# Kernel tuning notes

Hardware: AMD Instinct MI355X
Metric: run time of the kernel (lower is better)

Reference implementation:

```python
import jax, jax.numpy as jnp
import numpy as np

B, S, D, H = 2, 2048, 1024, 16
HD = D // H  # head_dim = 64


def setup_inputs() -> dict:
    key = jax.random.key(0)
    ks = jax.random.split(key, 12)
    xav = (2.0 / (D + D)) ** 0.5  # xavier_normal std for square Linear
    q = jax.random.normal(ks[0], (B, S, D), jnp.float32)
    k = jax.random.normal(ks[1], (B, S, D), jnp.float32)
    v = jax.random.normal(ks[2], (B, S, D), jnp.float32)
    Wq = jax.random.normal(ks[3], (D, D), jnp.float32) * xav
    Wk = jax.random.normal(ks[4], (D, D), jnp.float32) * xav
    Wv = jax.random.normal(ks[5], (D, D), jnp.float32) * xav
    bq = jnp.zeros((D,), jnp.float32)
    bk = jnp.zeros((D,), jnp.float32)
    bv = jnp.zeros((D,), jnp.float32)
    # valid-prefix padding masks (True = valid token); key 0 always valid so
    # no causal softmax row is fully masked (avoids NaN, matches real usage).
    klen = jax.random.randint(ks[6], (B,), S // 2, S + 1)
    qlen = jax.random.randint(ks[7], (B,), S // 2, S + 1)
    pos = jnp.arange(S)
    key_padding_mask = pos[None, :] < klen[:, None]
    query_padding_mask = pos[None, :] < qlen[:, None]
    return {
        "q": q, "k": k, "v": v,
        "Wq": Wq, "bq": bq, "Wk": Wk, "bk": bk, "Wv": Wv, "bv": bv,
        "key_padding_mask": key_padding_mask,
        "query_padding_mask": query_padding_mask,
    }


def _proj_split(x, W, b, n_heads):
    # Linear (y = x W^T + b) then split heads: [B,S,D] -> [B,H,S,hd]
    bsz, sq, dm = x.shape
    hd = dm // n_heads
    y = x @ W.T + b
    return y.reshape(bsz, sq, n_heads, hd).transpose(0, 2, 1, 3)


def reference(q, k, v, Wq, bq, Wk, bk, Wv, bv, key_padding_mask, query_padding_mask):
    bsz, sq, dm = q.shape
    sk = k.shape[1]
    Q = _proj_split(q, Wq, bq, H)  # [B,H,Sq,hd]
    K = _proj_split(k, Wk, bk, H)  # [B,H,Sk,hd]
    V = _proj_split(v, Wv, bv, H)  # [B,H,Sk,hd]
    scale = 1.0 / jnp.sqrt(jnp.asarray(Q.shape[-1], Q.dtype))
    scores = jnp.einsum('bhqd,bhkd->bhqk', Q, K) * scale  # [B,H,Sq,Sk]
    # key padding: -inf where key invalid
    scores = jnp.where(key_padding_mask[:, None, None, :], scores, -jnp.inf)
    # causal: -inf strictly above the diagonal
    causal_ok = jnp.tril(jnp.ones((sq, sk), bool))
    scores = jnp.where(causal_ok[None, None, :, :], scores, -jnp.inf)
    attn = jax.nn.softmax(scores, axis=-1)
    # q_mask: zero out rows for padded queries (post-softmax, as in source)
    attn = jnp.where(query_padding_mask[:, None, :, None], attn, 0.0)
    # dropout p=0.0 -> identity
    out = jnp.einsum('bhqk,bhkd->bhqd', attn, V)
    out = out.transpose(0, 2, 1, 3).reshape(bsz, sq, dm)
    return out + q
```

## Files before the change

kernel.cpp:

```cpp
#include <hip/hip_runtime.h>
#include <stdint.h>

#define BATCH 2
#define SEQ 2048
#define DMODEL 1024
#define NHEAD 16
#define HDIM 64
#define CVT_BLOCKS 15360

typedef __attribute__((ext_vector_type(8))) short bf16x8;
typedef __attribute__((ext_vector_type(4))) float f32x4;

__device__ __forceinline__ unsigned short f2bf(float f) {
  unsigned int u = __float_as_uint(f);
  u += 0x7fffu + ((u >> 16) & 1u);
  return (unsigned short)(u >> 16);
}
__device__ __forceinline__ unsigned int pk2bf(float a, float b) {
  return __builtin_amdgcn_perm(__float_as_uint(b) + 0x8000u,
                               __float_as_uint(a) + 0x8000u, 0x07060302u);
}
__device__ __forceinline__ void async_copy16(const void* g, void* l) {
  __builtin_amdgcn_global_load_lds(
      (const __attribute__((address_space(1))) void*)g,
      (__attribute__((address_space(3))) void*)l, 16, 0, 0);
}

__global__ __launch_bounds__(256) void cvt_all(
    const float* __restrict__ q, const float* __restrict__ k,
    const float* __restrict__ v, const float* __restrict__ Wq,
    const float* __restrict__ Wk, const float* __restrict__ Wv,
    unsigned short* __restrict__ dst,
    const unsigned char* __restrict__ kp, const unsigned char* __restrict__ qp,
    int* __restrict__ lens) {
  if (blockIdx.x == CVT_BLOCKS) {
    const int t = threadIdx.x, wave = t >> 6, lane = t & 63;
    const unsigned char* base = (wave < 2) ? kp : qp;
    const int b = wave & 1;
    const bool bytefmt = (base[1] != 0);
    int cnt = 0;
    if (bytefmt) {
      const uint4* p = (const uint4*)(base + (size_t)b * SEQ);
#pragma unroll
      for (int g = 0; g < 2; g++) {
        const uint4 x = p[g * 64 + lane];
        const unsigned int w[4] = {x.x, x.y, x.z, x.w};
#pragma unroll
        for (int i = 0; i < 4; i++) {
          const unsigned int ww = w[i];
          cnt += ((ww & 0xffu) != 0) + ((ww & 0xff00u) != 0) +
                 ((ww & 0xff0000u) != 0) + ((ww & 0xff000000u) != 0);
        }
      }
    } else {
      const uint4* p = (const uint4*)(base + (size_t)b * SEQ * 4);
#pragma unroll
      for (int g = 0; g < 8; g++) {
        const uint4 x = p[g * 64 + lane];
        cnt += (x.x != 0) + (x.y != 0) + (x.z != 0) + (x.w != 0);
      }
    }
#pragma unroll
    for (int off = 32; off >= 1; off >>= 1) cnt += __shfl_xor(cnt, off, 64);
    if (lane == 0) lens[wave] = cnt;
    return;
  }
  const int g = blockIdx.x * 256 + threadIdx.x;
  const float* src;
  size_t off, dbase;
  if (g < 3 * (1 << 20)) {
    const int ti = g >> 20;
    src = (ti == 0) ? q : (ti == 1) ? k : v;
    off = (size_t)(g & ((1 << 20) - 1));
    dbase = (size_t)ti << 22;
  } else {
    const int gw = g - 3 * (1 << 20);
    const int ti = gw >> 18;
    src = (ti == 0) ? Wq : (ti == 1) ? Wk : Wv;
    off = (size_t)(gw & ((1 << 18) - 1));
    dbase = (3ull << 22) + ((size_t)ti << 20);
  }
  const float4 x = ((const float4*)src)[off];
  ushort4 o;
  o.x = f2bf(x.x); o.y = f2bf(x.y); o.z = f2bf(x.z); o.w = f2bf(x.w);
  *(ushort4*)(dst + dbase + off * 4) = o;
}

__global__ __launch_bounds__(256) void qkv_proj(
    const unsigned short* __restrict__ xq, const unsigned short* __restrict__ xk,
    const unsigned short* __restrict__ xv,
    const unsigned short* __restrict__ Wq, const float* __restrict__ bq,
    const unsigned short* __restrict__ Wk, const float* __restrict__ bk,
    const unsigned short* __restrict__ Wv, const float* __restrict__ bv,
    unsigned short* __restrict__ Qo, unsigned short* __restrict__ Ko,
    unsigned short* __restrict__ Vo, const int* __restrict__ lens) {
  const int z = blockIdx.z;
  const int m0 = blockIdx.y * 128, n0 = blockIdx.x * 128;
  const int b = m0 >> 11;
  const int len = (z == 0) ? lens[2 + b] : lens[b];
  if ((m0 & (SEQ - 1)) >= len) return;

  const unsigned short* x = (z == 0) ? xq : (z == 1) ? xk : xv;
  const unsigned short* W = (z == 0) ? Wq : (z == 1) ? Wk : Wv;
  const float* bias = (z == 0) ? bq : (z == 1) ? bk : bv;
  unsigned short* dst = (z == 0) ? Qo : (z == 1) ? Ko : Vo;
  const float osc = (z == 0) ? 0.18033688011112042f : 1.0f;

  __shared__ unsigned short As[128 * 64];
  __shared__ unsigned short Bs[128 * 64];

  const int t = threadIdx.x;
  const int wave = t >> 6, lane = t & 63, quad = lane >> 4, l16 = lane & 15;
  const int wm = wave >> 1, wn = wave & 1;

  const f32x4 fz = {0.f, 0.f, 0.f, 0.f};
  f32x4 acc[4][4];
#pragma unroll
  for (int i = 0; i < 4; i++)
#pragma unroll
    for (int j = 0; j < 4; j++) acc[i][j] = fz;

  for (int k0 = 0; k0 < DMODEL; k0 += 64) {
    __syncthreads();
#pragma unroll
    for (int c = 0; c < 4; c++) {
      const int slot = c * 256 + t;
      const int row = slot >> 3, pg = slot & 7;
      const int lg = (pg ^ (row & 7)) * 8;
      async_copy16(x + (size_t)(m0 + row) * DMODEL + k0 + lg,
                   (char*)As + (c * 256 + (t & 192)) * 16);
      async_copy16(W + (size_t)(n0 + row) * DMODEL + k0 + lg,
                   (char*)Bs + (c * 256 + (t & 192)) * 16);
    }
    __syncthreads();
#pragma unroll
    for (int kk = 0; kk < 2; kk++) {
      bf16x8 af[4], bfr[4];
#pragma unroll
      for (int i = 0; i < 4; i++) {
        const int ra = wm * 64 + i * 16 + l16;
        const int rb = wn * 64 + i * 16 + l16;
        af[i] = *(const bf16x8*)(As + ra * 64 + ((kk * 4 + quad) ^ (ra & 7)) * 8);
        bfr[i] = *(const bf16x8*)(Bs + rb * 64 + ((kk * 4 + quad) ^ (rb & 7)) * 8);
      }
      if (z == 2) {
#pragma unroll
        for (int i = 0; i < 4; i++)
#pragma unroll
          for (int j = 0; j < 4; j++)
            acc[i][j] = __builtin_amdgcn_mfma_f32_16x16x32_bf16(af[i], bfr[j], acc[i][j], 0, 0, 0);
      } else {
#pragma unroll
        for (int i = 0; i < 4; i++)
#pragma unroll
          for (int j = 0; j < 4; j++)
            acc[i][j] = __builtin_amdgcn_mfma_f32_16x16x32_bf16(bfr[j], af[i], acc[i][j], 0, 0, 0);
      }
    }
  }

  if (z == 2) {
#pragma unroll
    for (int j = 0; j < 4; j++) {
      const int n = n0 + wn * 64 + j * 16 + l16;
      const float bb_ = bias[n];
      const int h = n >> 6, hd = n & 63;
#pragma unroll
      for (int i = 0; i < 4; i++) {
        const int s0 = (m0 & (SEQ - 1)) + wm * 64 + i * 16 + quad * 4;
        uint2 w;
        w.x = pk2bf(acc[i][j][0] + bb_, acc[i][j][1] + bb_);
        w.y = pk2bf(acc[i][j][2] + bb_, acc[i][j][3] + bb_);
        *(uint2*)(dst + (((size_t)(b * NHEAD + h) * HDIM + hd) << 11) + s0) = w;
      }
    }
  } else {
#pragma unroll
    for (int j = 0; j < 4; j++) {
      const int nb = n0 + wn * 64 + j * 16 + quad * 4;
      const float4 b4 = *(const float4*)(bias + nb);
      const int h = nb >> 6, hd0 = nb & 63;
#pragma unroll
      for (int i = 0; i < 4; i++) {
        const int s = (m0 & (SEQ - 1)) + wm * 64 + i * 16 + l16;
        uint2 w;
        w.x = pk2bf((acc[i][j][0] + b4.x) * osc, (acc[i][j][1] + b4.y) * osc);
        w.y = pk2bf((acc[i][j][2] + b4.z) * osc, (acc[i][j][3] + b4.w) * osc);
        *(uint2*)(dst + (((size_t)(b * NHEAD + h) * SEQ + s) << 6) + hd0) = w;
      }
    }
  }
}


template <bool MASKED>
__device__ __forceinline__ void softmax_update(
    const f32x4 s[8], int key0, int qrow, int klen, int quad, int l16,
    float& mst, float& lsum, f32x4 o[4], unsigned short* Pdst) {
  float pm[8][4];
  float rm = -__builtin_inff();
  if (MASKED) {
    const int kmax = ((qrow < klen - 1) ? qrow : klen - 1) - key0 - quad * 4;
#pragma unroll
    for (int nf = 0; nf < 8; nf++)
#pragma unroll
      for (int r = 0; r < 4; r++) {
        pm[nf][r] = (nf * 16 + r <= kmax) ? s[nf][r] : -__builtin_inff();
        rm = fmaxf(rm, pm[nf][r]);
      }
  } else {
#pragma unroll
    for (int nf = 0; nf < 8; nf++)
#pragma unroll
      for (int r = 0; r < 4; r++) {
        pm[nf][r] = s[nf][r];
        rm = fmaxf(rm, pm[nf][r]);
      }
  }
  rm = fmaxf(rm, __shfl_xor(rm, 16, 64));
  rm = fmaxf(rm, __shfl_xor(rm, 32, 64));
  if (__ballot(rm > mst) != 0ull) {
    const float mnew = fmaxf(mst, rm);
    const float alpha = exp2f(fmaxf(mst, -1e30f) - fmaxf(mnew, -1e30f));
    mst = mnew;
    lsum *= alpha;
    float ab[4];
#pragma unroll
    for (int r = 0; r < 4; r++) ab[r] = __shfl(alpha, quad * 4 + r, 64);
#pragma unroll
    for (int db = 0; db < 4; db++)
#pragma unroll
      for (int r = 0; r < 4; r++) o[db][r] *= ab[r];
  }
  const float mref = fmaxf(mst, -1e30f);
  float rs = 0.f;
#pragma unroll
  for (int nf = 0; nf < 8; nf++)
#pragma unroll
    for (int r = 0; r < 4; r++) {
      const float p = exp2f(pm[nf][r] - mref);
      pm[nf][r] = p;
      rs += p;
    }
  rs += __shfl_xor(rs, 16, 64);
  rs += __shfl_xor(rs, 32, 64);
  lsum += rs;
#pragma unroll
  for (int nf = 0; nf < 8; nf++) {
    uint2 w;
    w.x = pk2bf(pm[nf][0], pm[nf][1]);
    w.y = pk2bf(pm[nf][2], pm[nf][3]);
    const int grp = (nf * 2 + (quad >> 1)) ^ l16;
    *(uint2*)(Pdst + l16 * 128 + grp * 8 + (quad & 1) * 4) = w;
  }
}

template <bool MASKED>
__device__ __forceinline__ void tile_pass(
    const unsigned short* __restrict__ ks, const unsigned short* __restrict__ vt,
    unsigned short* __restrict__ Pw, bf16x8 qf0, bf16x8 qf1,
    int key0, int qrow, int klen, int quad, int l16,
    float& mst, float& lsum, f32x4 o[4]) {
  const f32x4 fz = {0.f, 0.f, 0.f, 0.f};
  f32x4 s[8];
#pragma unroll
  for (int nf = 0; nf < 8; nf++) {
    const int row = nf * 16 + l16;
    const int sw = row & 7;
    const bf16x8 kf0 = *(const bf16x8*)(ks + row * 64 + (quad ^ sw) * 8);
    const bf16x8 kf1 = *(const bf16x8*)(ks + row * 64 + ((quad + 4) ^ sw) * 8);
    f32x4 a = fz;
    a = __builtin_amdgcn_mfma_f32_16x16x32_bf16(kf0, qf0, a, 0, 0, 0);
    a = __builtin_amdgcn_mfma_f32_16x16x32_bf16(kf1, qf1, a, 0, 0, 0);
    s[nf] = a;
  }
  softmax_update<MASKED>(s, key0, qrow, klen, quad, l16, mst, lsum, o, Pw);
  bf16x8 pf[4];
#pragma unroll
  for (int ksn = 0; ksn < 4; ksn++)
    pf[ksn] = *(const bf16x8*)(Pw + l16 * 128 + ((ksn * 4 + quad) ^ l16) * 8);
#pragma unroll
  for (int db = 0; db < 4; db++) {
    const int d = db * 16 + l16;
#pragma unroll
    for (int ksn = 0; ksn < 4; ksn++) {
      const bf16x8 v = *(const bf16x8*)(vt + d * 128 + ((ksn * 4 + quad) ^ l16) * 8);
      o[db] = __builtin_amdgcn_mfma_f32_16x16x32_bf16(pf[ksn], v, o[db], 0, 0, 0);
    }
  }
}

__global__ __launch_bounds__(512, 4) void attn_kernel(
    const unsigned short* __restrict__ Qb, const unsigned short* __restrict__ Kb,
    const unsigned short* __restrict__ VTb, const float* __restrict__ qin,
    const int* __restrict__ lens, float* __restrict__ out) {
  const int pi = blockIdx.x, h = blockIdx.y, b = blockIdx.z;
  const int bh = b * NHEAD + h;
  const int t = threadIdx.x, wave = t >> 6, lane = t & 63, quad = lane >> 4, l16 = lane & 15;
  const int grp = wave >> 2, w4 = wave & 3;
  const int lo = pi, hi = 31 - pi;
  const int myTile = grp ? hi : lo;
  const int klen = lens[b], qlen = lens[2 + b];

  __shared__ unsigned short Ks[128 * 64];
  __shared__ unsigned short VT[64 * 128];
  __shared__ unsigned short Ps[8][16 * 128];

  const unsigned short* Qp = Qb + (size_t)bh * SEQ * HDIM;
  const unsigned short* Kp = Kb + (size_t)bh * SEQ * HDIM;
  const unsigned short* Vt = VTb + (size_t)bh * HDIM * SEQ;

  const int qrow = myTile * 64 + w4 * 16 + l16;
  const bf16x8 qf0 = *(const bf16x8*)(Qp + (size_t)qrow * HDIM + quad * 8);
  const bf16x8 qf1 = *(const bf16x8*)(Qp + (size_t)qrow * HDIM + 32 + quad * 8);

  const f32x4 fz = {0.f, 0.f, 0.f, 0.f};
  f32x4 o[4];
#pragma unroll
  for (int i = 0; i < 4; i++) o[i] = fz;
  float mst = -__builtin_inff(), lsum = 0.f;

  const int kendLO = ((lo * 64 + 64) < klen) ? (lo * 64 + 64) : klen;
  const int ktotLO = (kendLO + 127) >> 7;
  int ktotHI = 0;
  if (hi * 64 < qlen) {
    const int kendHI = ((hi * 64 + 64) < klen) ? (hi * 64 + 64) : klen;
    ktotHI = (kendHI + 127) >> 7;
  }
  const int ktot = (ktotHI > ktotLO) ? ktotHI : ktotLO;
  const int myktot = grp ? ktotHI : ktotLO;

  for (int kt = 0; kt < ktot; kt++) {
    const int key0 = kt << 7;
    __syncthreads();
#pragma unroll
    for (int c = 0; c < 2; c++) {
      const int slot = c * 512 + t;
      const int row = slot >> 3, pg = slot & 7;
      async_copy16(Kp + (size_t)(key0 + row) * HDIM + (pg ^ (row & 7)) * 8,
                   (char*)Ks + (c * 512 + (t & 448)) * 16);
    }
#pragma unroll
    for (int c = 0; c < 2; c++) {
      const int slot = c * 512 + t;
      const int row = slot >> 4, pg = slot & 15;
      async_copy16(Vt + (size_t)row * SEQ + key0 + (pg ^ (row & 15)) * 8,
                   (char*)VT + (c * 512 + (t & 448)) * 16);
    }
    __syncthreads();

    if (kt < myktot) {
      if ((key0 + 127 <= myTile * 64) && (key0 + 127 < klen))
        tile_pass<false>(Ks, VT, Ps[wave], qf0, qf1, key0, qrow, klen, quad, l16, mst, lsum, o);
      else
        tile_pass<true>(Ks, VT, Ps[wave], qf0, qf1, key0, qrow, klen, quad, l16, mst, lsum, o);
    }
  }

  const float inv = (lsum > 0.f) ? 1.f / lsum : 0.f;
  float ib[4];
#pragma unroll
  for (int r = 0; r < 4; r++) ib[r] = __shfl(inv, quad * 4 + r, 64);
#pragma unroll
  for (int db = 0; db < 4; db++) {
    const int col = h * HDIM + db * 16 + l16;
#pragma unroll
    for (int r = 0; r < 4; r++) {
      const int i = myTile * 64 + w4 * 16 + quad * 4 + r;
      const size_t oo = (size_t)(b * SEQ + i) * DMODEL + col;
      out[oo] = ((i < qlen) ? o[db][r] * ib[r] : 0.f) + qin[oo];
    }
  }
}

extern "C" void kernel_launch(void* const* d_in, const int* in_sizes, int n_in,
                              void* d_out, int out_size, void* d_ws, size_t ws_size,
                              hipStream_t stream) {
  (void)in_sizes; (void)n_in; (void)out_size; (void)ws_size;
  const float* q = (const float*)d_in[0];
  const float* k = (const float*)d_in[1];
  const float* v = (const float*)d_in[2];
  const float* Wq = (const float*)d_in[3];
  const float* bq = (const float*)d_in[4];
  const float* Wk = (const float*)d_in[5];
  const float* bk = (const float*)d_in[6];
  const float* Wv = (const float*)d_in[7];
  const float* bv = (const float*)d_in[8];
  const unsigned char* kpm = (const unsigned char*)d_in[9];
  const unsigned char* qpm = (const unsigned char*)d_in[10];
  float* out = (float*)d_out;

  const size_t tsz = (size_t)BATCH * SEQ * DMODEL;
  const size_t wsz = (size_t)DMODEL * DMODEL;

  char* ws = (char*)d_ws;
  int* lens = (int*)ws;
  unsigned short* cvt_base = (unsigned short*)(ws + 256);
  unsigned short* qb16 = cvt_base;
  unsigned short* kb16 = qb16 + tsz;
  unsigned short* vb16 = kb16 + tsz;
  unsigned short* Wqb = vb16 + tsz;
  unsigned short* Wkb = Wqb + wsz;
  unsigned short* Wvb = Wkb + wsz;
  unsigned short* Qw = Wvb + wsz;
  unsigned short* Kw = Qw + tsz;
  unsigned short* Vtw = Kw + tsz;

  cvt_all<<<dim3(CVT_BLOCKS + 1), dim3(256), 0, stream>>>(q, k, v, Wq, Wk, Wv,
                                                          cvt_base, kpm, qpm, lens);
  qkv_proj<<<dim3(8, 32, 3), dim3(256), 0, stream>>>(qb16, kb16, vb16, Wqb, bq, Wkb, bk, Wvb, bv, Qw, Kw, Vtw, lens);
  attn_kernel<<<dim3(16, NHEAD, BATCH), dim3(512), 0, stream>>>(Qw, Kw, Vtw, q, lens, out);
}
```

Measured before the change: 210.0 us.

## Double-buffer 64-key K/V tiles in attention loop with async prefetch

Halves the key tile from 128 to 64 keys and double-buffers K and V in shared memory, so the next tile's async global-to-LDS copy is issued before the current tile is computed. This removes one barrier per iteration and aims to hide load latency. It also skips fully masked work more finely (per-wave causal bound, LO group needs only lo+1 tiles), adds s_setprio around the MFMA sections, and lowers the launch-bounds occupancy hint from 4 to 2. The trade-off is more loop iterations and barriers per key, and possibly lower occupancy.

```diff
diff --git a/kernel.cpp b/kernel.cpp
--- a/kernel.cpp
+++ b/kernel.cpp
@@ -193,16 +193,18 @@
 }
 
 
+#define KVB 64
+
 template <bool MASKED>
 __device__ __forceinline__ void softmax_update(
-    const f32x4 s[8], int key0, int qrow, int klen, int quad, int l16,
+    const f32x4 s[4], int key0, int qrow, int klen, int quad, int l16,
     float& mst, float& lsum, f32x4 o[4], unsigned short* Pdst) {
-  float pm[8][4];
+  float pm[4][4];
   float rm = -__builtin_inff();
   if (MASKED) {
     const int kmax = ((qrow < klen - 1) ? qrow : klen - 1) - key0 - quad * 4;
 #pragma unroll
-    for (int nf = 0; nf < 8; nf++)
+    for (int nf = 0; nf < 4; nf++)
 #pragma unroll
       for (int r = 0; r < 4; r++) {
         pm[nf][r] = (nf * 16 + r <= kmax) ? s[nf][r] : -__builtin_inff();
@@ -210,7 +212,7 @@
       }
   } else {
 #pragma unroll
-    for (int nf = 0; nf < 8; nf++)
+    for (int nf = 0; nf < 4; nf++)
 #pragma unroll
       for (int r = 0; r < 4; r++) {
         pm[nf][r] = s[nf][r];
@@ -235,7 +237,7 @@
   const float mref = fmaxf(mst, -1e30f);
   float rs = 0.f;
 #pragma unroll
-  for (int nf = 0; nf < 8; nf++)
+  for (int nf = 0; nf < 4; nf++)
 #pragma unroll
     for (int r = 0; r < 4; r++) {
       const float p = exp2f(pm[nf][r] - mref);
@@ -246,12 +248,12 @@
   rs += __shfl_xor(rs, 32, 64);
   lsum += rs;
 #pragma unroll
-  for (int nf = 0; nf < 8; nf++) {
+  for (int nf = 0; nf < 4; nf++) {
     uint2 w;
     w.x = pk2bf(pm[nf][0], pm[nf][1]);
     w.y = pk2bf(pm[nf][2], pm[nf][3]);
-    const int grp = (nf * 2 + (quad >> 1)) ^ l16;
-    *(uint2*)(Pdst + l16 * 128 + grp * 8 + (quad & 1) * 4) = w;
+    const int g = (nf * 2 + (quad >> 1)) ^ (l16 & 7);
+    *(uint2*)(Pdst + l16 * KVB + g * 8 + (quad & 1) * 4) = w;
   }
 }
 
@@ -262,9 +264,10 @@
     int key0, int qrow, int klen, int quad, int l16,
     float& mst, float& lsum, f32x4 o[4]) {
   const f32x4 fz = {0.f, 0.f, 0.f, 0.f};
-  f32x4 s[8];
-#pragma unroll
-  for (int nf = 0; nf < 8; nf++) {
+  f32x4 s[4];
+  __builtin_amdgcn_s_setprio(1);
+#pragma unroll
+  for (int nf = 0; nf < 4; nf++) {
     const int row = nf * 16 + l16;
     const int sw = row & 7;
     const bf16x8 kf0 = *(const bf16x8*)(ks + row * 64 + (quad ^ sw) * 8);
@@ -274,23 +277,27 @@
     a = __builtin_amdgcn_mfma_f32_16x16x32_bf16(kf1, qf1, a, 0, 0, 0);
     s[nf] = a;
   }
+  __builtin_amdgcn_s_setprio(0);
   softmax_update<MASKED>(s, key0, qrow, klen, quad, l16, mst, lsum, o, Pw);
-  bf16x8 pf[4];
-#pragma unroll
-  for (int ksn = 0; ksn < 4; ksn++)
-    pf[ksn] = *(const bf16x8*)(Pw + l16 * 128 + ((ksn * 4 + quad) ^ l16) * 8);
+  bf16x8 pf[2];
+#pragma unroll
+  for (int ksn = 0; ksn < 2; ksn++)
+    pf[ksn] = *(const bf16x8*)(Pw + l16 * KVB + ((ksn * 4 + quad) ^ (l16 & 7)) * 8);
+  __builtin_amdgcn_s_setprio(1);
 #pragma unroll
   for (int db = 0; db < 4; db++) {
     const int d = db * 16 + l16;
-#pragma unroll
-    for (int ksn = 0; ksn < 4; ksn++) {
-      const bf16x8 v = *(const bf16x8*)(vt + d * 128 + ((ksn * 4 + quad) ^ l16) * 8);
+    const int sw = d & 7;
+#pragma unroll
+    for (int ksn = 0; ksn < 2; ksn++) {
+      const bf16x8 v = *(const bf16x8*)(vt + d * KVB + ((ksn * 4 + quad) ^ sw) * 8);
       o[db] = __builtin_amdgcn_mfma_f32_16x16x32_bf16(pf[ksn], v, o[db], 0, 0, 0);
     }
   }
-}
-
-__global__ __launch_bounds__(512, 4) void attn_kernel(
+  __builtin_amdgcn_s_setprio(0);
+}
+
+__global__ __launch_bounds__(512, 2) void attn_kernel(
     const unsigned short* __restrict__ Qb, const unsigned short* __restrict__ Kb,
     const unsigned short* __restrict__ VTb, const float* __restrict__ qin,
     const int* __restrict__ lens, float* __restrict__ out) {
@@ -302,9 +309,9 @@
   const int myTile = grp ? hi : lo;
   const int klen = lens[b], qlen = lens[2 + b];
 
-  __shared__ unsigned short Ks[128 * 64];
-  __shared__ unsigned short VT[64 * 128];
-  __shared__ unsigned short Ps[8][16 * 128];
+  __shared__ unsigned short Ks[2][KVB * 64];
+  __shared__ unsigned short VT[2][KVB * 64];
+  __shared__ unsigned short Ps[8][16 * KVB];
 
   const unsigned short* Qp = Qb + (size_t)bh * SEQ * HDIM;
   const unsigned short* Kp = Kb + (size_t)bh * SEQ * HDIM;
@@ -320,41 +327,41 @@
   for (int i = 0; i < 4; i++) o[i] = fz;
   float mst = -__builtin_inff(), lsum = 0.f;
 
-  const int kendLO = ((lo * 64 + 64) < klen) ? (lo * 64 + 64) : klen;
-  const int ktotLO = (kendLO + 127) >> 7;
-  int ktotHI = 0;
+  const int ktLO = lo + 1;
+  int ktHI = 0;
   if (hi * 64 < qlen) {
     const int kendHI = ((hi * 64 + 64) < klen) ? (hi * 64 + 64) : klen;
-    ktotHI = (kendHI + 127) >> 7;
-  }
-  const int ktot = (ktotHI > ktotLO) ? ktotHI : ktotLO;
-  const int myktot = grp ? ktotHI : ktotLO;
-
+    ktHI = (kendHI + 63) >> 6;
+  }
+  const int ktot = (ktLO > ktHI) ? ktLO : ktHI;
+  const int myt = grp ? ktHI : ktLO;
+
+  auto STAGE = [&](int buf, int kt) {
+    const int key0 = kt << 6;
+    const int row = t >> 3;
+    const int sg = ((t & 7) ^ (row & 7)) * 8;
+    async_copy16(Kp + (size_t)(key0 + row) * HDIM + sg,
+                 (char*)Ks[buf] + (t & 448) * 16);
+    async_copy16(Vt + (size_t)row * SEQ + key0 + sg,
+                 (char*)VT[buf] + (t & 448) * 16);
+  };
+
+  STAGE(0, 0);
+  __syncthreads();
+  int cur = 0;
   for (int kt = 0; kt < ktot; kt++) {
-    const int key0 = kt << 7;
+    if (kt + 1 < ktot) STAGE(cur ^ 1, kt + 1);
+    if (kt < myt) {
+      const int key0 = kt << 6;
+      if ((key0 + 63 <= myTile * 64 + w4 * 16) && (key0 + 63 < klen))
+        tile_pass<false>(Ks[cur], VT[cur], Ps[wave], qf0, qf1, key0, qrow,
+                         klen, quad, l16, mst, lsum, o);
+      else
+        tile_pass<true>(Ks[cur], VT[cur], Ps[wave], qf0, qf1, key0, qrow,
+                        klen, quad, l16, mst, lsum, o);
+    }
     __syncthreads();
-#pragma unroll
-    for (int c = 0; c < 2; c++) {
-      const int slot = c * 512 + t;
-      const int row = slot >> 3, pg = slot & 7;
-      async_copy16(Kp + (size_t)(key0 + row) * HDIM + (pg ^ (row & 7)) * 8,
-                   (char*)Ks + (c * 512 + (t & 448)) * 16);
-    }
-#pragma unroll
-    for (int c = 0; c < 2; c++) {
-      const int slot = c * 512 + t;
-      const int row = slot >> 4, pg = slot & 15;
-      async_copy16(Vt + (size_t)row * SEQ + key0 + (pg ^ (row & 15)) * 8,
-                   (char*)VT + (c * 512 + (t & 448)) * 16);
-    }
-    __syncthreads();
-
-    if (kt < myktot) {
-      if ((key0 + 127 <= myTile * 64) && (key0 + 127 < klen))
-        tile_pass<false>(Ks, VT, Ps[wave], qf0, qf1, key0, qrow, klen, quad, l16, mst, lsum, o);
-      else
-        tile_pass<true>(Ks, VT, Ps[wave], qf0, qf1, key0, qrow, klen, quad, l16, mst, lsum, o);
-    }
+    cur ^= 1;
   }
 
   const float inv = (lsum > 0.f) ? 1.f / lsum : 0.f;
```

Result: no change. 206.1 us (-1.8%).
